# Optimization experiments

Hardware: AMD Instinct MI355X
Metric: run time of the kernel (lower is better)

The kernel has to match this reference:

```python
import jax, jax.numpy as jnp
import numpy as np

DIM = 512
NUM_HEADS = 8


def setup_inputs() -> dict:
    key = jax.random.key(0)
    ks = jax.random.split(key, 9)
    B, C, H, W = 8, DIM, 32, 32
    s = 1.0 / np.sqrt(DIM)  # conv-style init scale
    return {
        "x": jax.random.normal(ks[0], (B, C, H, W), jnp.float32),
        "Wq": jax.random.normal(ks[1], (DIM, DIM), jnp.float32) * s,
        "bq": jnp.zeros((DIM,), jnp.float32),
        "Wk": jax.random.normal(ks[2], (DIM, DIM), jnp.float32) * s,
        "bk": jnp.zeros((DIM,), jnp.float32),
        "Wv": jax.random.normal(ks[3], (DIM, DIM), jnp.float32) * s,
        "bv": jnp.zeros((DIM,), jnp.float32),
        "Wo": jax.random.normal(ks[4], (DIM, DIM), jnp.float32) * s,
        "bo": jnp.zeros((DIM,), jnp.float32),
    }


def _proj(x, W, b):
    # 1x1 conv == per-pixel linear over channels: [out_c, in_c] x [b, in_c, h, w]
    return jnp.einsum('oc,bchw->bohw', W, x) + b[None, :, None, None]


def reference(x, Wq, bq, Wk, bk, Wv, bv, Wo, bo):
    b, c, h, w = x.shape
    g = NUM_HEADS
    dh = c // g  # per-head channels
    q = _proj(x, Wq, bq)
    k = _proj(x, Wk, bk)
    v = _proj(x, Wv, bv)
    # 'b (g c) h w -> (b g) c (h w)'
    def split_heads(t):
        return t.reshape(b, g, dh, h * w).reshape(b * g, dh, h * w)
    q, k, v = split_heads(q), split_heads(k), split_heads(v)
    # note: scale uses full dim (as in the source), not per-head dim
    a = jnp.einsum('bcs,bct->bst', q, k) / jnp.sqrt(jnp.float32(c))
    a = jax.nn.softmax(a, axis=-1)  # dropout is identity at inference
    o = jnp.einsum('bst,bct->bcs', a, v)  # [(b g), dh, s]
    o = o.reshape(b, g * dh, h, w)  # '(b g) c (h w) -> b (g c) h w'
    return x + _proj(o, Wo, bo)
```

## Files before the change

### kernel.cpp

```cpp
#include <hip/hip_runtime.h>

typedef unsigned short u16;
typedef __attribute__((ext_vector_type(8))) short short8;
typedef __attribute__((ext_vector_type(4))) short sh4;
typedef __attribute__((ext_vector_type(2))) int int2v;
typedef __attribute__((ext_vector_type(4))) float floatx4;

__device__ __forceinline__ float b2f(u16 u) {
  unsigned int x = ((unsigned int)u) << 16;
  return __builtin_bit_cast(float, x);
}
__device__ __forceinline__ u16 f2b(float f) {
  unsigned int x = __builtin_bit_cast(unsigned int, f);
  unsigned int r = (x + 0x7FFFu + ((x >> 16) & 1u)) >> 16;
  return (u16)r;
}
__device__ __forceinline__ unsigned int pk2bf(float a, float b) {
  unsigned int ua = __builtin_bit_cast(unsigned int, a) + 0x8000u;
  unsigned int ub = __builtin_bit_cast(unsigned int, b) + 0x8000u;
  return __builtin_amdgcn_perm(ub, ua, 0x07060302u);
}

#if __has_builtin(__builtin_amdgcn_mfma_f32_16x16x16bf16_1k)
#define MFMA16(a, b, c) __builtin_amdgcn_mfma_f32_16x16x16bf16_1k((a), (b), (c), 0, 0, 0)
#define MFMA16_DRAIN()
#else
__device__ __forceinline__ floatx4 mfma16_fb(sh4 a, sh4 b, floatx4 c) {
  asm volatile("s_nop 1\n\tv_mfma_f32_16x16x16_bf16 %0, %1, %2, %0"
               : "+v"(c) : "v"(a), "v"(b));
  return c;
}
#define MFMA16(a, b, c) mfma16_fb((a), (b), (c))
#define MFMA16_DRAIN() asm volatile("s_nop 7\n\ts_nop 7\n\ts_nop 7")
#endif

#if __has_builtin(__builtin_amdgcn_exp2f)
#define EXP2F(x) __builtin_amdgcn_exp2f(x)
#else
#define EXP2F(x) __expf((x) * 0.6931471805599453f)
#endif

#define MFMA32(a, b, c) __builtin_amdgcn_mfma_f32_16x16x32_bf16((a), (b), (c), 0, 0, 0)

#define GLL16(g, l) __builtin_amdgcn_global_load_lds(                         \
    (const __attribute__((address_space(1))) unsigned int*)(g),               \
    (__attribute__((address_space(3))) unsigned int*)(l), 16, 0, 0)

#define SC_LOG2E 0.06375872f

__device__ __forceinline__ int detect_fp32(const u16* __restrict__ x) {
  __shared__ int cnt;
  if (threadIdx.x == 0) cnt = 0;
  __syncthreads();
  int c = 0;
  if (threadIdx.x < 256) {
#pragma unroll
    for (int i = 0; i < 16; ++i) {
      u16 u = x[threadIdx.x * 16 + i];
      if (((u >> 7) & 0xFF) >= 0xC8) c++;
    }
  }
  if (c) atomicAdd(&cnt, c);
  __syncthreads();
  return cnt > 32;
}

__global__ __launch_bounds__(256) void prep(
    const u16* __restrict__ x,
    const u16* w0, const u16* w1, const u16* w2, const u16* w3,
    const u16* c0, const u16* c1, const u16* c2, const u16* c3,
    u16* __restrict__ xT, u16* __restrict__ Wc, u16* __restrict__ bc, int b0) {
  const int fp32 = detect_fp32(x);
  const int tid = threadIdx.x;
  if (blockIdx.y < 8) {
    __shared__ u16 t[64][65];
    const int lb = blockIdx.z, b = b0 + lb;
    const int p0 = blockIdx.x * 64, cc0 = blockIdx.y * 64;
    const int tx = tid & 63, ty = tid >> 6;
    if (fp32) {
      const float* xb = (const float*)x + (long)b * 524288;
#pragma unroll
      for (int i = 0; i < 16; ++i) {
        int c = ty + i * 4;
        t[c][tx] = f2b(xb[(long)(cc0 + c) * 1024 + p0 + tx]);
      }
    } else {
      const u16* xb = x + (long)b * 524288;
#pragma unroll
      for (int i = 0; i < 16; ++i) {
        int c = ty + i * 4;
        t[c][tx] = xb[(long)(cc0 + c) * 1024 + p0 + tx];
      }
    }
    __syncthreads();
    u16* xTb = xT + (long)lb * 524288;
#pragma unroll
    for (int i = 0; i < 16; ++i) {
      int p = ty + i * 4;
      xTb[(long)(p0 + p) * 512 + cc0 + tx] = t[tx][p];
    }
  } else {
    const u16* srcs[8] = {w0, w1, w2, w3, c0, c1, c2, c3};
    const int nthreads = gridDim.z * 16 * 256;
    const int flat = (blockIdx.z * 16 + blockIdx.x) * 256 + tid;
    for (int vi = flat; vi < 131072; vi += nthreads) {
      int w = vi >> 15;
      int off = (vi & 32767) * 8;
      u16* dst = Wc + w * 262144 + off;
      if (fp32) {
        const float* s = (const float*)srcs[w] + off;
        u16 tmp[8];
#pragma unroll
        for (int r = 0; r < 8; ++r) tmp[r] = f2b(s[r]);
        *(int4*)dst = *(const int4*)tmp;
      } else {
        *(int4*)dst = *(const int4*)(srcs[w] + off);
      }
    }
    for (int gi = flat; gi < 2048; gi += nthreads) {
      int t2 = gi >> 9;
      bc[gi] = fp32 ? f2b(((const float*)srcs[4 + t2])[gi & 511]) : srcs[4 + t2][gi & 511];
    }
  }
}

struct GemmLds3 {
  u16 As[3][128][32], Bs[3][128][32];
};

__global__ __launch_bounds__(512, 4) void gemm_qkv(
    const u16* __restrict__ xT, const u16* __restrict__ Wc,
    const u16* __restrict__ bc, u16* __restrict__ Qt, u16* __restrict__ Kt,
    u16* __restrict__ Vv) {
  __shared__ GemmLds3 lds;
  const long bz = blockIdx.x;
  const u16* xb = xT + bz * 524288;
  const int bx = blockIdx.y;
  const int qk = bx < 64;
  const int t = qk ? bx : bx - 64;
  const int m0 = (t >> 3) * 128, n0 = (t & 7) * 128;
  const u16* A = qk ? xb : (Wc + 524288);
  const u16* B = qk ? Wc : xb;

  const int tid = threadIdx.x;
  const int wave = tid >> 6, lane = tid & 63;
  const int quad = lane >> 4, l15 = lane & 15;
  const int wm = (wave >> 1) * 32, wn = (wave & 1) * 64;
  const int lrow = lane >> 2, lcol = (lane & 3) * 8;
  const int ra = wave * 16;

  floatx4 acc[2][4] = {};

#define QKV_STAGE(bufi, k0)                                                   \
  {                                                                           \
    GLL16(A + (long)(m0 + ra + lrow) * 512 + (k0) + lcol,                     \
          &lds.As[bufi][ra][0]);                                              \
    GLL16(B + (long)(n0 + ra + lrow) * 512 + (k0) + lcol,                     \
          &lds.Bs[bufi][ra][0]);                                              \
  }

  QKV_STAGE(0, 0);
  int buf = 0, nbuf = 1;
  for (int i = 0; i < 16; ++i) {
    if (i < 15) {
      QKV_STAGE(nbuf, (i + 1) * 32);
      asm volatile("s_waitcnt vmcnt(2)" ::: "memory");
    } else {
      asm volatile("s_waitcnt vmcnt(0)" ::: "memory");
    }
    __builtin_amdgcn_s_barrier();
    __builtin_amdgcn_sched_barrier(0);
    short8 af[2], bf[4];
#pragma unroll
    for (int ii = 0; ii < 2; ++ii)
      af[ii] = *(const short8*)&lds.As[buf][wm + ii * 16 + l15][quad * 8];
#pragma unroll
    for (int j = 0; j < 4; ++j)
      bf[j] = *(const short8*)&lds.Bs[buf][wn + j * 16 + l15][quad * 8];
#pragma unroll
    for (int ii = 0; ii < 2; ++ii)
#pragma unroll
      for (int j = 0; j < 4; ++j)
        acc[ii][j] = MFMA32(af[ii], bf[j], acc[ii][j]);
    buf = nbuf;
    nbuf = nbuf == 2 ? 0 : nbuf + 1;
  }
#undef QKV_STAGE

  if (qk) {
    u16* Qz = Qt + bz * 524288;
    u16* Kz = Kt + bz * 524288;
#pragma unroll
    for (int i = 0; i < 2; ++i)
#pragma unroll
      for (int j = 0; j < 4; ++j)
#pragma unroll
        for (int r = 0; r < 4; ++r) {
          int gm = m0 + wm + i * 16 + quad * 4 + r;
          int gn = n0 + wn + j * 16 + l15;
          float v = acc[i][j][r] + b2f(bc[gn]);
          if (gn < 512) Qz[(long)gm * 512 + gn] = f2b(v * SC_LOG2E);
          else Kz[(long)gm * 512 + gn - 512] = f2b(v);
        }
  } else {
    u16* Vz = Vv + bz * 524288;
    const u16* bv = bc + 1024;
#pragma unroll
    for (int i = 0; i < 2; ++i)
#pragma unroll
      for (int j = 0; j < 4; ++j)
#pragma unroll
        for (int r = 0; r < 4; ++r) {
          int gm = m0 + wm + i * 16 + quad * 4 + r;
          int gn = n0 + wn + j * 16 + l15;
          float v = acc[i][j][r] + b2f(bv[gm]);
          Vz[(long)gm * 1024 + gn] = f2b(v);
        }
  }
}

struct OutLds3 {
  u16 As[3][128][32], Bs[3][64][32];
};

__global__ __launch_bounds__(256) void gemm_out(
    const u16* __restrict__ Wo, const u16* __restrict__ bo,
    const u16* __restrict__ Ow, const u16* __restrict__ xraw,
    u16* __restrict__ out) {
  const int fp32 = detect_fp32(xraw);
  __shared__ OutLds3 lds;
  const long bz = blockIdx.x;
  const u16* B = Ow + bz * 524288;
  const int m0 = blockIdx.z * 128, n0 = blockIdx.y * 64;
  const int tid = threadIdx.x;
  const int wave = tid >> 6, lane = tid & 63;
  const int quad = lane >> 4, l15 = lane & 15;
  const int lrow = lane >> 2, lcol = (lane & 3) * 8;

  floatx4 acc[2][4] = {};

#define OUT_STAGE3(bufi, k0)                                                  \
  {                                                                           \
    const int ra = wave * 32;                                                 \
    GLL16(Wo + (long)(m0 + ra + lrow) * 512 + (k0) + lcol,                    \
          &lds.As[bufi][ra][0]);                                              \
    GLL16(Wo + (long)(m0 + ra + 16 + lrow) * 512 + (k0) + lcol,               \
          &lds.As[bufi][ra + 16][0]);                                         \
    GLL16(B + (long)(n0 + wave * 16 + lrow) * 512 + (k0) + lcol,              \
          &lds.Bs[bufi][wave * 16][0]);                                       \
  }

  OUT_STAGE3(0, 0);
  int buf = 0, nbuf = 1;
  for (int i = 0; i < 16; ++i) {
    if (i < 15) {
      OUT_STAGE3(nbuf, (i + 1) * 32);
      asm volatile("s_waitcnt vmcnt(3)" ::: "memory");
    } else {
      asm volatile("s_waitcnt vmcnt(0)" ::: "memory");
    }
    __builtin_amdgcn_s_barrier();
    __builtin_amdgcn_sched_barrier(0);
#pragma unroll
    for (int ii = 0; ii < 2; ++ii) {
      short8 af = *(const short8*)&lds.As[buf][wave * 32 + ii * 16 + l15][quad * 8];
#pragma unroll
      for (int j = 0; j < 4; ++j) {
        short8 bf = *(const short8*)&lds.Bs[buf][j * 16 + l15][quad * 8];
        acc[ii][j] = MFMA32(af, bf, acc[ii][j]);
      }
    }
    buf = nbuf;
    nbuf = nbuf == 2 ? 0 : nbuf + 1;
  }
#undef OUT_STAGE3

#pragma unroll
  for (int i = 0; i < 2; ++i)
#pragma unroll
    for (int j = 0; j < 4; ++j)
#pragma unroll
      for (int r = 0; r < 4; ++r) {
        int gm = m0 + wave * 32 + i * 16 + quad * 4 + r;
        int gn = n0 + j * 16 + l15;
        float v = acc[i][j][r] + b2f(bo[gm]);
        long idx = bz * 524288 + (long)gm * 1024 + gn;
        if (fp32) {
          v += ((const float*)xraw)[idx];
          ((float*)out)[idx] = v;
        } else {
          v += b2f(xraw[idx]);
          out[idx] = f2b(v);
        }
      }
}

#define AP 72
__global__ __launch_bounds__(256, 2) void attn(
    const u16* __restrict__ Qt, const u16* __restrict__ Kt,
    const u16* __restrict__ V, u16* __restrict__ O) {
  __shared__ alignas(16) u16 Ks[2][64][AP];
  __shared__ alignas(16) u16 Vs[2][64][AP];
  const int bg = blockIdx.x;
  const int lb = bg >> 3, head = bg & 7;
  const int s0 = blockIdx.y * 128;
  const int tid = threadIdx.x;
  const int wave = tid >> 6, lane = tid & 63;
  const int quad = lane >> 4, l15 = lane & 15;

  const u16* Qb = Qt + (long)lb * 524288 + head * 64;
  const u16* Kb = Kt + (long)lb * 524288 + head * 64;
  const u16* Vb = V + (long)(lb * 512 + head * 64) * 1024;
  u16* Ob = O + (long)lb * 524288 + head * 64;

  short8 bq[2][2];
#pragma unroll
  for (int qb = 0; qb < 2; ++qb)
#pragma unroll
    for (int kk = 0; kk < 2; ++kk)
      bq[qb][kk] = *(const short8*)&Qb[(long)(s0 + wave * 32 + qb * 16 + l15) * 512 +
                                       kk * 32 + quad * 8];

  const int r0 = tid >> 3, o0 = (tid & 7) * 8;
  int4 kreg0, kreg1, vreg0, vreg1;
  kreg0 = *(const int4*)&Kb[(long)r0 * 512 + o0];
  kreg1 = *(const int4*)&Kb[(long)(r0 + 32) * 512 + o0];
  vreg0 = *(const int4*)&Vb[(long)r0 * 1024 + o0];
  vreg1 = *(const int4*)&Vb[(long)(r0 + 32) * 1024 + o0];
  *(int4*)&Ks[0][r0][o0] = kreg0;
  *(int4*)&Ks[0][r0 + 32][o0] = kreg1;
  *(int4*)&Vs[0][r0][o0] = vreg0;
  *(int4*)&Vs[0][r0 + 32][o0] = vreg1;

  floatx4 acc[2][4] = {};
  floatx4 accl[2] = {};
  const sh4 ones = {(short)0x3F80, (short)0x3F80, (short)0x3F80, (short)0x3F80};

  for (int it16 = 0; it16 < 16; ++it16) {
    const int buf = it16 & 1;
    const int t0n = (it16 + 1) * 64;
    if (it16 < 15) {
      kreg0 = *(const int4*)&Kb[(long)(t0n + r0) * 512 + o0];
      kreg1 = *(const int4*)&Kb[(long)(t0n + r0 + 32) * 512 + o0];
      vreg0 = *(const int4*)&Vb[(long)r0 * 1024 + t0n + o0];
      vreg1 = *(const int4*)&Vb[(long)(r0 + 32) * 1024 + t0n + o0];
    }
    __syncthreads();

    floatx4 p[2][4] = {};
#pragma unroll
    for (int kk = 0; kk < 2; ++kk) {
      short8 ak[4];
#pragma unroll
      for (int mi = 0; mi < 4; ++mi)
        ak[mi] = *(const short8*)&Ks[buf][mi * 16 + l15][kk * 32 + quad * 8];
#pragma unroll
      for (int qb = 0; qb < 2; ++qb)
#pragma unroll
        for (int mi = 0; mi < 4; ++mi)
          p[qb][mi] = MFMA32(ak[mi], bq[qb][kk], p[qb][mi]);
    }

    sh4 pk[2][4];
#pragma unroll
    for (int qb = 0; qb < 2; ++qb)
#pragma unroll
      for (int mi = 0; mi < 4; ++mi) {
        float e0 = EXP2F(p[qb][mi][0]);
        float e1 = EXP2F(p[qb][mi][1]);
        float e2 = EXP2F(p[qb][mi][2]);
        float e3 = EXP2F(p[qb][mi][3]);
        int2v w;
        w.x = (int)pk2bf(e0, e1);
        w.y = (int)pk2bf(e2, e3);
        pk[qb][mi] = __builtin_bit_cast(sh4, w);
      }

#pragma unroll
    for (int qb = 0; qb < 2; ++qb)
#pragma unroll
      for (int mi = 0; mi < 4; ++mi) accl[qb] = MFMA16(ones, pk[qb][mi], accl[qb]);

#pragma unroll
    for (int mi = 0; mi < 4; ++mi) {
      sh4 av[4];
#pragma unroll
      for (int ci = 0; ci < 4; ++ci)
        av[ci] = *(const sh4*)&Vs[buf][ci * 16 + l15][mi * 16 + quad * 4];
#pragma unroll
      for (int qb = 0; qb < 2; ++qb)
#pragma unroll
        for (int ci = 0; ci < 4; ++ci)
          acc[qb][ci] = MFMA16(av[ci], pk[qb][mi], acc[qb][ci]);
    }

    if (it16 < 15) {
      const int nb = 1 - buf;
      *(int4*)&Ks[nb][r0][o0] = kreg0;
      *(int4*)&Ks[nb][r0 + 32][o0] = kreg1;
      *(int4*)&Vs[nb][r0][o0] = vreg0;
      *(int4*)&Vs[nb][r0 + 32][o0] = vreg1;
    }
  }
  MFMA16_DRAIN();

  const float inv0 = 1.0f / accl[0][0];
  const float inv1 = 1.0f / accl[1][0];

  u16 (*Os)[AP] = (u16(*)[AP]) & Ks[0][0][0];
  __syncthreads();
#pragma unroll
  for (int qb = 0; qb < 2; ++qb) {
    const float inv = qb ? inv1 : inv0;
#pragma unroll
    for (int ci = 0; ci < 4; ++ci) {
      int2v w;
      w.x = (int)pk2bf(acc[qb][ci][0] * inv, acc[qb][ci][1] * inv);
      w.y = (int)pk2bf(acc[qb][ci][2] * inv, acc[qb][ci][3] * inv);
      *(int2v*)&Os[wave * 32 + qb * 16 + l15][ci * 16 + quad * 4] = w;
    }
  }
  __syncthreads();
  {
    const int srow = tid >> 1, cb = (tid & 1) * 32;
#pragma unroll
    for (int c = 0; c < 32; c += 8)
      *(int4*)&Ob[(long)(s0 + srow) * 512 + cb + c] = *(const int4*)&Os[srow][cb + c];
  }
}

extern "C" void kernel_launch(void* const* d_in, const int* in_sizes, int n_in,
                              void* d_out, int out_size, void* d_ws, size_t ws_size,
                              hipStream_t stream) {
  const u16* x  = (const u16*)d_in[0];
  const u16* Wq = (const u16*)d_in[1];
  const u16* bq = (const u16*)d_in[2];
  const u16* Wk = (const u16*)d_in[3];
  const u16* bk = (const u16*)d_in[4];
  const u16* Wv = (const u16*)d_in[5];
  const u16* bv = (const u16*)d_in[6];
  const u16* Wo = (const u16*)d_in[7];
  const u16* bo = (const u16*)d_in[8];
  u16* out = (u16*)d_out;
  u16* ws = (u16*)d_ws;

  const size_t PLAN_A_BYTES = 27267072;

  if (ws_size >= PLAN_A_BYTES) {
    u16* xT = ws;
    u16* Kt = ws + 4194304;
    u16* Vv = ws + 8388608;
    u16* Wc = ws + 12582912;
    u16* bc = ws + 13631488;
    u16* Qt = out;
    u16* Ow = xT;

    prep<<<dim3(16, 9, 8), 256, 0, stream>>>(x, Wq, Wk, Wv, Wo,
                                             bq, bk, bv, bo, xT, Wc, bc, 0);
    gemm_qkv<<<dim3(8, 96), 512, 0, stream>>>(xT, Wc, bc, Qt, Kt, Vv);
    attn<<<dim3(64, 8), 256, 0, stream>>>(Qt, Kt, Vv, Ow);
    gemm_out<<<dim3(8, 16, 4), 256, 0, stream>>>(Wc + 786432, bc + 1536, Ow, x, out);
  } else {
    u16* Ow = ws;
    u16* Kt = ws + 4194304;
    u16* Vv = ws + 6291456;
    u16* Wc = ws + 8388608;
    u16* bc = ws + 9437184;
    u16* Qt = out;

    for (int phase = 0; phase < 2; ++phase) {
      const int b0 = phase * 4;
      u16* xT = Ow + (long)phase * 2097152;
      prep<<<dim3(16, 9, 4), 256, 0, stream>>>(x, Wq, Wk, Wv, Wo,
                                               bq, bk, bv, bo, xT, Wc, bc, b0);
      gemm_qkv<<<dim3(4, 96), 512, 0, stream>>>(xT, Wc, bc, Qt, Kt, Vv);
      attn<<<dim3(32, 8), 256, 0, stream>>>(Qt, Kt, Vv, Ow + (long)b0 * 524288);
    }
    gemm_out<<<dim3(8, 16, 4), 256, 0, stream>>>(Wc + 786432, bc + 1536, Ow, x, out);
  }
}
```

Baseline: 157.0 us.

## Load QKV GEMM fragments directly from global memory into registers, skipping LDS

The QKV projection GEMM no longer stages A/B tiles through shared memory with global-to-LDS loads and barriers. Each wave now reads its MFMA operand fragments straight from global memory into registers, double-buffered in software. The block tile shrinks to 128x64 with 4 waves, which doubles the grid. This removes LDS traffic and barrier stalls, but each wave fetches its own B fragments and loses cross-wave reuse, so it leans on L2/L1 bandwidth with uncoalesced 16-byte row reads.

Result: slower. 212.3 us (+35.3%).

```diff
diff --git a/kernel.cpp b/kernel.cpp
--- a/kernel.cpp
+++ b/kernel.cpp
@@ -124,68 +124,62 @@
   }
 }
 
-struct GemmLds3 {
-  u16 As[3][128][32], Bs[3][128][32];
-};
-
-__global__ __launch_bounds__(512, 4) void gemm_qkv(
+__device__ __forceinline__ void qkv_mfma8(const short8 (&aa)[2],
+                                          const short8 (&bb)[4],
+                                          floatx4 (&acc)[2][4]) {
+#pragma unroll
+  for (int ii = 0; ii < 2; ++ii)
+#pragma unroll
+    for (int j = 0; j < 4; ++j)
+      acc[ii][j] = MFMA32(aa[ii], bb[j], acc[ii][j]);
+}
+
+__global__ __launch_bounds__(256, 4) void gemm_qkv(
     const u16* __restrict__ xT, const u16* __restrict__ Wc,
     const u16* __restrict__ bc, u16* __restrict__ Qt, u16* __restrict__ Kt,
     u16* __restrict__ Vv) {
-  __shared__ GemmLds3 lds;
   const long bz = blockIdx.x;
   const u16* xb = xT + bz * 524288;
-  const int bx = blockIdx.y;
-  const int qk = bx < 64;
-  const int t = qk ? bx : bx - 64;
-  const int m0 = (t >> 3) * 128, n0 = (t & 7) * 128;
+  const int ty = blockIdx.y;
+  const int qk = ty < 128;
+  const int t = qk ? ty : ty - 128;
+  const int m0 = (t >> 4) * 128, n0 = (t & 15) * 64;
   const u16* A = qk ? xb : (Wc + 524288);
   const u16* B = qk ? Wc : xb;
 
   const int tid = threadIdx.x;
   const int wave = tid >> 6, lane = tid & 63;
   const int quad = lane >> 4, l15 = lane & 15;
-  const int wm = (wave >> 1) * 32, wn = (wave & 1) * 64;
-  const int lrow = lane >> 2, lcol = (lane & 3) * 8;
-  const int ra = wave * 16;
+  const int q8 = quad * 8;
+  const int wm = wave * 32;
+
+  const u16* Ar0 = A + (long)(m0 + wm + l15) * 512 + q8;
+  const u16* Ar1 = A + (long)(m0 + wm + 16 + l15) * 512 + q8;
+  const u16* Br0 = B + (long)(n0 + l15) * 512 + q8;
+  const u16* Br1 = Br0 + 16 * 512;
+  const u16* Br2 = Br0 + 32 * 512;
+  const u16* Br3 = Br0 + 48 * 512;
 
   floatx4 acc[2][4] = {};
-
-#define QKV_STAGE(bufi, k0)                                                   \
-  {                                                                           \
-    GLL16(A + (long)(m0 + ra + lrow) * 512 + (k0) + lcol,                     \
-          &lds.As[bufi][ra][0]);                                              \
-    GLL16(B + (long)(n0 + ra + lrow) * 512 + (k0) + lcol,                     \
-          &lds.Bs[bufi][ra][0]);                                              \
-  }
-
-  QKV_STAGE(0, 0);
-  int buf = 0, nbuf = 1;
-  for (int i = 0; i < 16; ++i) {
-    if (i < 15) {
-      QKV_STAGE(nbuf, (i + 1) * 32);
-      asm volatile("s_waitcnt vmcnt(2)" ::: "memory");
-    } else {
-      asm volatile("s_waitcnt vmcnt(0)" ::: "memory");
-    }
-    __builtin_amdgcn_s_barrier();
-    __builtin_amdgcn_sched_barrier(0);
-    short8 af[2], bf[4];
-#pragma unroll
-    for (int ii = 0; ii < 2; ++ii)
-      af[ii] = *(const short8*)&lds.As[buf][wm + ii * 16 + l15][quad * 8];
-#pragma unroll
-    for (int j = 0; j < 4; ++j)
-      bf[j] = *(const short8*)&lds.Bs[buf][wn + j * 16 + l15][quad * 8];
-#pragma unroll
-    for (int ii = 0; ii < 2; ++ii)
-#pragma unroll
-      for (int j = 0; j < 4; ++j)
-        acc[ii][j] = MFMA32(af[ii], bf[j], acc[ii][j]);
-    buf = nbuf;
-    nbuf = nbuf == 2 ? 0 : nbuf + 1;
-  }
-#undef QKV_STAGE
+  short8 a0[2], b0[4], a1[2], b1[4];
+
+#define QLOAD(aa, bb, k0)                                                     \
+  aa[0] = *(const short8*)(Ar0 + (k0));                                       \
+  aa[1] = *(const short8*)(Ar1 + (k0));                                       \
+  bb[0] = *(const short8*)(Br0 + (k0));                                       \
+  bb[1] = *(const short8*)(Br1 + (k0));                                       \
+  bb[2] = *(const short8*)(Br2 + (k0));                                       \
+  bb[3] = *(const short8*)(Br3 + (k0));
+
+  QLOAD(a0, b0, 0);
+#pragma unroll
+  for (int k = 0; k < 512; k += 64) {
+    QLOAD(a1, b1, k + 32);
+    qkv_mfma8(a0, b0, acc);
+    if (k + 64 < 512) QLOAD(a0, b0, k + 64);
+    qkv_mfma8(a1, b1, acc);
+  }
+#undef QLOAD
 
   if (qk) {
     u16* Qz = Qt + bz * 524288;
@@ -197,7 +191,7 @@
 #pragma unroll
         for (int r = 0; r < 4; ++r) {
           int gm = m0 + wm + i * 16 + quad * 4 + r;
-          int gn = n0 + wn + j * 16 + l15;
+          int gn = n0 + j * 16 + l15;
           float v = acc[i][j][r] + b2f(bc[gn]);
           if (gn < 512) Qz[(long)gm * 512 + gn] = f2b(v * SC_LOG2E);
           else Kz[(long)gm * 512 + gn - 512] = f2b(v);
@@ -212,7 +206,7 @@
 #pragma unroll
         for (int r = 0; r < 4; ++r) {
           int gm = m0 + wm + i * 16 + quad * 4 + r;
-          int gn = n0 + wn + j * 16 + l15;
+          int gn = n0 + j * 16 + l15;
           float v = acc[i][j][r] + b2f(bv[gm]);
           Vz[(long)gm * 1024 + gn] = f2b(v);
         }
@@ -457,7 +451,7 @@
 
     prep<<<dim3(16, 9, 8), 256, 0, stream>>>(x, Wq, Wk, Wv, Wo,
                                              bq, bk, bv, bo, xT, Wc, bc, 0);
-    gemm_qkv<<<dim3(8, 96), 512, 0, stream>>>(xT, Wc, bc, Qt, Kt, Vv);
+    gemm_qkv<<<dim3(8, 192), 256, 0, stream>>>(xT, Wc, bc, Qt, Kt, Vv);
     attn<<<dim3(64, 8), 256, 0, stream>>>(Qt, Kt, Vv, Ow);
     gemm_out<<<dim3(8, 16, 4), 256, 0, stream>>>(Wc + 786432, bc + 1536, Ow, x, out);
   } else {
@@ -473,7 +467,7 @@
       u16* xT = Ow + (long)phase * 2097152;
       prep<<<dim3(16, 9, 4), 256, 0, stream>>>(x, Wq, Wk, Wv, Wo,
                                                bq, bk, bv, bo, xT, Wc, bc, b0);
-      gemm_qkv<<<dim3(4, 96), 512, 0, stream>>>(xT, Wc, bc, Qt, Kt, Vv);
+      gemm_qkv<<<dim3(4, 192), 256, 0, stream>>>(xT, Wc, bc, Qt, Kt, Vv);
       attn<<<dim3(32, 8), 256, 0, stream>>>(Qt, Kt, Vv, Ow + (long)b0 * 524288);
     }
     gemm_out<<<dim3(8, 16, 4), 256, 0, stream>>>(Wc + 786432, bc + 1536, Ow, x, out);
```

## Shrink GEMM tiles to 64x64, prefetch two stages ahead, prioritize attention MFMA

Applied to the files above, without the earlier changes.

Both projection GEMMs now use 64x64 tiles with 256-thread blocks, which raises the block count (qkv 768→3072, out 512→1024) for better CU fill. The load pipeline now issues two stages ahead and places the next-next load after the barrier. The attention kernel also wraps its MFMA sections in s_setprio to favour matrix issue. Smaller tiles reduce operand reuse and increase global/LDS traffic per flop.

After: 160.5 us. 2.3% more time.

```diff
diff --git a/kernel.cpp b/kernel.cpp
--- a/kernel.cpp
+++ b/kernel.cpp
@@ -124,32 +124,32 @@
   }
 }
 
-struct GemmLds3 {
-  u16 As[3][128][32], Bs[3][128][32];
+struct QkvLds {
+  u16 As[3][64][32], Bs[3][64][32];
 };
 
-__global__ __launch_bounds__(512, 4) void gemm_qkv(
+__global__ __launch_bounds__(256) void gemm_qkv(
     const u16* __restrict__ xT, const u16* __restrict__ Wc,
     const u16* __restrict__ bc, u16* __restrict__ Qt, u16* __restrict__ Kt,
     u16* __restrict__ Vv) {
-  __shared__ GemmLds3 lds;
+  __shared__ QkvLds lds;
   const long bz = blockIdx.x;
   const u16* xb = xT + bz * 524288;
-  const int bx = blockIdx.y;
-  const int qk = bx < 64;
-  const int t = qk ? bx : bx - 64;
-  const int m0 = (t >> 3) * 128, n0 = (t & 7) * 128;
+  const int ty = blockIdx.y;
+  const int qk = ty < 256;
+  const int t = qk ? ty : ty - 256;
+  const int m0 = (t >> 4) * 64, n0 = (t & 15) * 64;
   const u16* A = qk ? xb : (Wc + 524288);
   const u16* B = qk ? Wc : xb;
 
   const int tid = threadIdx.x;
   const int wave = tid >> 6, lane = tid & 63;
   const int quad = lane >> 4, l15 = lane & 15;
-  const int wm = (wave >> 1) * 32, wn = (wave & 1) * 64;
+  const int wm = (wave >> 1) * 32, wn = (wave & 1) * 32;
   const int lrow = lane >> 2, lcol = (lane & 3) * 8;
   const int ra = wave * 16;
 
-  floatx4 acc[2][4] = {};
+  floatx4 acc[2][2] = {};
 
 #define QKV_STAGE(bufi, k0)                                                   \
   {                                                                           \
@@ -160,30 +160,31 @@
   }
 
   QKV_STAGE(0, 0);
-  int buf = 0, nbuf = 1;
+  QKV_STAGE(1, 32);
+  int buf = 0, nbuf2 = 2;
   for (int i = 0; i < 16; ++i) {
     if (i < 15) {
-      QKV_STAGE(nbuf, (i + 1) * 32);
       asm volatile("s_waitcnt vmcnt(2)" ::: "memory");
     } else {
       asm volatile("s_waitcnt vmcnt(0)" ::: "memory");
     }
     __builtin_amdgcn_s_barrier();
     __builtin_amdgcn_sched_barrier(0);
-    short8 af[2], bf[4];
+    if (i + 2 < 16) QKV_STAGE(nbuf2, (i + 2) * 32);
+    short8 af[2], bf[2];
 #pragma unroll
     for (int ii = 0; ii < 2; ++ii)
       af[ii] = *(const short8*)&lds.As[buf][wm + ii * 16 + l15][quad * 8];
 #pragma unroll
-    for (int j = 0; j < 4; ++j)
+    for (int j = 0; j < 2; ++j)
       bf[j] = *(const short8*)&lds.Bs[buf][wn + j * 16 + l15][quad * 8];
 #pragma unroll
     for (int ii = 0; ii < 2; ++ii)
 #pragma unroll
-      for (int j = 0; j < 4; ++j)
+      for (int j = 0; j < 2; ++j)
         acc[ii][j] = MFMA32(af[ii], bf[j], acc[ii][j]);
-    buf = nbuf;
-    nbuf = nbuf == 2 ? 0 : nbuf + 1;
+    buf = buf == 2 ? 0 : buf + 1;
+    nbuf2 = nbuf2 == 2 ? 0 : nbuf2 + 1;
   }
 #undef QKV_STAGE
 
@@ -193,7 +194,7 @@
 #pragma unroll
     for (int i = 0; i < 2; ++i)
 #pragma unroll
-      for (int j = 0; j < 4; ++j)
+      for (int j = 0; j < 2; ++j)
 #pragma unroll
         for (int r = 0; r < 4; ++r) {
           int gm = m0 + wm + i * 16 + quad * 4 + r;
@@ -208,7 +209,7 @@
 #pragma unroll
     for (int i = 0; i < 2; ++i)
 #pragma unroll
-      for (int j = 0; j < 4; ++j)
+      for (int j = 0; j < 2; ++j)
 #pragma unroll
         for (int r = 0; r < 4; ++r) {
           int gm = m0 + wm + i * 16 + quad * 4 + r;
@@ -219,8 +220,8 @@
   }
 }
 
-struct OutLds3 {
-  u16 As[3][128][32], Bs[3][64][32];
+struct OutLdsS {
+  u16 As[3][64][32], Bs[3][64][32];
 };
 
 __global__ __launch_bounds__(256) void gemm_out(
@@ -228,61 +229,64 @@
     const u16* __restrict__ Ow, const u16* __restrict__ xraw,
     u16* __restrict__ out) {
   const int fp32 = detect_fp32(xraw);
-  __shared__ OutLds3 lds;
+  __shared__ OutLdsS lds;
   const long bz = blockIdx.x;
   const u16* B = Ow + bz * 524288;
-  const int m0 = blockIdx.z * 128, n0 = blockIdx.y * 64;
+  const int m0 = blockIdx.z * 64, n0 = blockIdx.y * 64;
   const int tid = threadIdx.x;
   const int wave = tid >> 6, lane = tid & 63;
   const int quad = lane >> 4, l15 = lane & 15;
+  const int wm = (wave >> 1) * 32, wn = (wave & 1) * 32;
   const int lrow = lane >> 2, lcol = (lane & 3) * 8;
-
-  floatx4 acc[2][4] = {};
-
-#define OUT_STAGE3(bufi, k0)                                                  \
+  const int ra = wave * 16;
+
+  floatx4 acc[2][2] = {};
+
+#define OUT_STAGE(bufi, k0)                                                   \
   {                                                                           \
-    const int ra = wave * 32;                                                 \
     GLL16(Wo + (long)(m0 + ra + lrow) * 512 + (k0) + lcol,                    \
           &lds.As[bufi][ra][0]);                                              \
-    GLL16(Wo + (long)(m0 + ra + 16 + lrow) * 512 + (k0) + lcol,               \
-          &lds.As[bufi][ra + 16][0]);                                         \
-    GLL16(B + (long)(n0 + wave * 16 + lrow) * 512 + (k0) + lcol,              \
-          &lds.Bs[bufi][wave * 16][0]);                                       \
-  }
-
-  OUT_STAGE3(0, 0);
-  int buf = 0, nbuf = 1;
+    GLL16(B + (long)(n0 + ra + lrow) * 512 + (k0) + lcol,                     \
+          &lds.Bs[bufi][ra][0]);                                              \
+  }
+
+  OUT_STAGE(0, 0);
+  OUT_STAGE(1, 32);
+  int buf = 0, nbuf2 = 2;
   for (int i = 0; i < 16; ++i) {
     if (i < 15) {
-      OUT_STAGE3(nbuf, (i + 1) * 32);
-      asm volatile("s_waitcnt vmcnt(3)" ::: "memory");
+      asm volatile("s_waitcnt vmcnt(2)" ::: "memory");
     } else {
       asm volatile("s_waitcnt vmcnt(0)" ::: "memory");
     }
     __builtin_amdgcn_s_barrier();
     __builtin_amdgcn_sched_barrier(0);
-#pragma unroll
-    for (int ii = 0; ii < 2; ++ii) {
-      short8 af = *(const short8*)&lds.As[buf][wave * 32 + ii * 16 + l15][quad * 8];
-#pragma unroll
-      for (int j = 0; j < 4; ++j) {
-        short8 bf = *(const short8*)&lds.Bs[buf][j * 16 + l15][quad * 8];
-        acc[ii][j] = MFMA32(af, bf, acc[ii][j]);
-      }
-    }
-    buf = nbuf;
-    nbuf = nbuf == 2 ? 0 : nbuf + 1;
-  }
-#undef OUT_STAGE3
+    if (i + 2 < 16) OUT_STAGE(nbuf2, (i + 2) * 32);
+    short8 af[2], bf[2];
+#pragma unroll
+    for (int ii = 0; ii < 2; ++ii)
+      af[ii] = *(const short8*)&lds.As[buf][wm + ii * 16 + l15][quad * 8];
+#pragma unroll
+    for (int j = 0; j < 2; ++j)
+      bf[j] = *(const short8*)&lds.Bs[buf][wn + j * 16 + l15][quad * 8];
+#pragma unroll
+    for (int ii = 0; ii < 2; ++ii)
+#pragma unroll
+      for (int j = 0; j < 2; ++j)
+        acc[ii][j] = MFMA32(af[ii], bf[j], acc[ii][j]);
+    buf = buf == 2 ? 0 : buf + 1;
+    nbuf2 = nbuf2 == 2 ? 0 : nbuf2 + 1;
+  }
+#undef OUT_STAGE
 
 #pragma unroll
   for (int i = 0; i < 2; ++i)
 #pragma unroll
-    for (int j = 0; j < 4; ++j)
+    for (int j = 0; j < 2; ++j)
 #pragma unroll
       for (int r = 0; r < 4; ++r) {
-        int gm = m0 + wave * 32 + i * 16 + quad * 4 + r;
-        int gn = n0 + j * 16 + l15;
+        int gm = m0 + wm + i * 16 + quad * 4 + r;
+        int gn = n0 + wn + j * 16 + l15;
         float v = acc[i][j][r] + b2f(bo[gm]);
         long idx = bz * 524288 + (long)gm * 1024 + gn;
         if (fp32) {
@@ -354,11 +358,13 @@
 #pragma unroll
       for (int mi = 0; mi < 4; ++mi)
         ak[mi] = *(const short8*)&Ks[buf][mi * 16 + l15][kk * 32 + quad * 8];
+      __builtin_amdgcn_s_setprio(1);
 #pragma unroll
       for (int qb = 0; qb < 2; ++qb)
 #pragma unroll
         for (int mi = 0; mi < 4; ++mi)
           p[qb][mi] = MFMA32(ak[mi], bq[qb][kk], p[qb][mi]);
+      __builtin_amdgcn_s_setprio(0);
     }
 
     sh4 pk[2][4];
@@ -381,6 +387,7 @@
 #pragma unroll
       for (int mi = 0; mi < 4; ++mi) accl[qb] = MFMA16(ones, pk[qb][mi], accl[qb]);
 
+    __builtin_amdgcn_s_setprio(1);
 #pragma unroll
     for (int mi = 0; mi < 4; ++mi) {
       sh4 av[4];
@@ -393,6 +400,7 @@
         for (int ci = 0; ci < 4; ++ci)
           acc[qb][ci] = MFMA16(av[ci], pk[qb][mi], acc[qb][ci]);
     }
+    __builtin_amdgcn_s_setprio(0);
 
     if (it16 < 15) {
       const int nb = 1 - buf;
@@ -457,9 +465,9 @@
 
     prep<<<dim3(16, 9, 8), 256, 0, stream>>>(x, Wq, Wk, Wv, Wo,
                                              bq, bk, bv, bo, xT, Wc, bc, 0);
-    gemm_qkv<<<dim3(8, 96), 512, 0, stream>>>(xT, Wc, bc, Qt, Kt, Vv);
+    gemm_qkv<<<dim3(8, 384), 256, 0, stream>>>(xT, Wc, bc, Qt, Kt, Vv);
     attn<<<dim3(64, 8), 256, 0, stream>>>(Qt, Kt, Vv, Ow);
-    gemm_out<<<dim3(8, 16, 4), 256, 0, stream>>>(Wc + 786432, bc + 1536, Ow, x, out);
+    gemm_out<<<dim3(8, 16, 8), 256, 0, stream>>>(Wc + 786432, bc + 1536, Ow, x, out);
   } else {
     u16* Ow = ws;
     u16* Kt = ws + 4194304;
@@ -473,9 +481,9 @@
       u16* xT = Ow + (long)phase * 2097152;
       prep<<<dim3(16, 9, 4), 256, 0, stream>>>(x, Wq, Wk, Wv, Wo,
                                                bq, bk, bv, bo, xT, Wc, bc, b0);
-      gemm_qkv<<<dim3(4, 96), 512, 0, stream>>>(xT, Wc, bc, Qt, Kt, Vv);
+      gemm_qkv<<<dim3(4, 384), 256, 0, stream>>>(xT, Wc, bc, Qt, Kt, Vv);
       attn<<<dim3(32, 8), 256, 0, stream>>>(Qt, Kt, Vv, Ow + (long)b0 * 524288);
     }
-    gemm_out<<<dim3(8, 16, 4), 256, 0, stream>>>(Wc + 786432, bc + 1536, Ow, x, out);
-  }
-}
+    gemm_out<<<dim3(8, 16, 8), 256, 0, stream>>>(Wc + 786432, bc + 1536, Ow, x, out);
+  }
+}
```
